# Performance work log

Measured on AMD Instinct MI355X. Metric: run time of the kernel, lower is better.

The kernel has to match this reference:

```python
import jax, jax.numpy as jnp
import numpy as np

B, S, H, K = 64, 512, 768, 21  # batch, seq_len, bert hidden, num_labels


def setup_inputs() -> dict:
    key = jax.random.key(0)
    ks = jax.random.split(key, 8)
    hidden = jax.random.normal(ks[0], (B, S, H), jnp.float32)  # post-BERT states
    W = jax.random.normal(ks[1], (H, K), jnp.float32) * 0.02    # classifier weight
    b = jnp.zeros((K,), jnp.float32)                            # classifier bias
    start_transitions = jax.random.uniform(ks[2], (K,), jnp.float32, -0.1, 0.1)
    transitions = jax.random.uniform(ks[3], (K, K), jnp.float32, -0.1, 0.1)
    end_transitions = jax.random.uniform(ks[4], (K,), jnp.float32, -0.1, 0.1)
    labels = jax.random.randint(ks[5], (B, S), 0, K)
    # torchcrf requires mask[:, 0] == 1; use variable-length prefix masks
    lengths = jax.random.randint(ks[6], (B,), S // 2, S + 1)
    attention_mask = jnp.arange(S)[None, :] < lengths[:, None]  # [B,S] bool
    return dict(hidden=hidden, W=W, b=b,
                start_transitions=start_transitions,
                transitions=transitions,
                end_transitions=end_transitions,
                labels=labels, attention_mask=attention_mask)


def _crf_nll(logits, labels, mask, start_t, trans, end_t):
    """torchcrf CRF forward (reduction='sum' log-likelihood), negated."""
    fmask = mask.astype(logits.dtype)  # [B,S]
    # ---- numerator: score of the gold path ----
    emit = jnp.take_along_axis(logits, labels[..., None], axis=2)[..., 0]  # [B,S]
    tr = trans[labels[:, :-1], labels[:, 1:]]                              # [B,S-1]
    num = start_t[labels[:, 0]] + emit[:, 0] \
        + jnp.sum((emit[:, 1:] + tr) * fmask[:, 1:], axis=1)
    lengths = mask.sum(axis=1)
    last_tags = jnp.take_along_axis(labels, (lengths - 1)[:, None], axis=1)[:, 0]
    num = num + end_t[last_tags]
    # ---- denominator: forward algorithm (logsumexp recurrence) ----
    alpha0 = start_t[None, :] + logits[:, 0]           # [B,K]
    ems = jnp.swapaxes(logits[:, 1:], 0, 1)            # [S-1,B,K]
    ms = jnp.swapaxes(mask[:, 1:], 0, 1)               # [S-1,B]

    def step(alpha, xs):
        em, m = xs
        nxt = jax.scipy.special.logsumexp(
            alpha[:, :, None] + trans[None, :, :] + em[:, None, :], axis=1)
        return jnp.where(m[:, None], nxt, alpha), None

    alpha, _ = jax.lax.scan(step, alpha0, (ems, ms))
    logZ = jax.scipy.special.logsumexp(alpha + end_t[None, :], axis=1)  # [B]
    return jnp.sum(logZ - num)  # negative log-likelihood (sum over batch)


def reference(hidden, W, b, start_transitions, transitions, end_transitions,
              labels, attention_mask):
    # dropout is identity in eval; the GRU in __init__ is unused in forward
    logits = hidden @ W + b  # [B,S,K]
    nll = _crf_nll(logits, labels, attention_mask,
                   start_transitions, transitions, end_transitions)
    # module returns (logits, -1 * log_likelihood) = (logits, nll)
    return (logits, nll)
```

## Files before the change

kernel.cpp:

```cpp
#include <hip/hip_runtime.h>

#define BSZ 64
#define SEQ 512
#define HID 768
#define NK  21
#define NSEG 32
#define SEGLEN 16
#define PSTR 448

typedef short bf16x8 __attribute__((ext_vector_type(8)));
typedef float f32x4  __attribute__((ext_vector_type(4)));

__device__ __forceinline__ unsigned f2bf1(float x) {
    unsigned u = __float_as_uint(x);
    return (u + 0x7fffu + ((u >> 16) & 1u)) >> 16;
}
__device__ __forceinline__ unsigned f2bf_pk(float lo, float hi) {
    return f2bf1(lo) | (f2bf1(hi) << 16);
}
__device__ __forceinline__ float bf2f(unsigned short v) {
    return __uint_as_float(((unsigned)v) << 16);
}

__global__ __launch_bounds__(256) void wconv_len_kernel(
    const float* __restrict__ W, const int* __restrict__ mask,
    unsigned short* __restrict__ WT, int* __restrict__ Lbuf)
{
    if (blockIdx.x < 96) {
        const int idx = blockIdx.x * 256 + threadIdx.x;
        const int n = idx / HID;
        const int k = idx - n * HID;
        unsigned short v = 0;
        if (n < NK) v = (unsigned short)f2bf1(W[(size_t)k * NK + n]);
        WT[idx] = v;
    } else {
        const int tid = threadIdx.x;
        const int b = tid >> 2, q = tid & 3;
        const int* msk = mask + b * SEQ + q * 128;
        int cnt = 0;
        for (int r = 0; r < 128; ++r) cnt += (msk[r] != 0);
        cnt += __shfl_xor(cnt, 1, 64);
        cnt += __shfl_xor(cnt, 2, 64);
        if (q == 0) Lbuf[b] = cnt;
    }
}

__global__ __launch_bounds__(256) void gemm_bias_kernel(
    const float* __restrict__ hidden, const unsigned short* __restrict__ WT,
    const float* __restrict__ bias, float* __restrict__ out)
{
    const int tid  = threadIdx.x;
    const int lane = tid & 63;
    const int wv   = tid >> 6;
    const int n    = lane & 15;
    const int quad = lane >> 4;

    const int arow = blockIdx.x * 64 + wv * 16 + n;
    const float* ap = hidden + (size_t)arow * HID + quad * 8;
    const bf16x8* bp0 = (const bf16x8*)(WT + (size_t)n * HID + quad * 8);
    const bf16x8* bp1 = (const bf16x8*)(WT + (size_t)(16 + n) * HID + quad * 8);

    f32x4 acc0 = {0.f, 0.f, 0.f, 0.f};
    f32x4 acc1 = {0.f, 0.f, 0.f, 0.f};

    float4 c0a = *(const float4*)(ap + 0);
    float4 c0b = *(const float4*)(ap + 4);

    #pragma unroll
    for (int c = 0; c < HID / 32; ++c) {
        float4 c1a, c1b;
        if (c + 1 < HID / 32) {
            c1a = *(const float4*)(ap + (c + 1) * 32);
            c1b = *(const float4*)(ap + (c + 1) * 32 + 4);
        }
        union { bf16x8 v; unsigned u[4]; } af;
        af.u[0] = f2bf_pk(c0a.x, c0a.y);
        af.u[1] = f2bf_pk(c0a.z, c0a.w);
        af.u[2] = f2bf_pk(c0b.x, c0b.y);
        af.u[3] = f2bf_pk(c0b.z, c0b.w);

        const bf16x8 b0 = bp0[c * 4];
        const bf16x8 b1 = bp1[c * 4];

        acc0 = __builtin_amdgcn_mfma_f32_16x16x32_bf16(af.v, b0, acc0, 0, 0, 0);
        acc1 = __builtin_amdgcn_mfma_f32_16x16x32_bf16(af.v, b1, acc1, 0, 0, 0);
        c0a = c1a; c0b = c1b;
    }

    const float b0v = bias[n];
    const float b1v = (n < NK - 16) ? bias[16 + n] : 0.f;
    const int rbase = blockIdx.x * 64 + wv * 16 + quad * 4;
    #pragma unroll
    for (int r = 0; r < 4; ++r) {
        float* op = out + (size_t)(rbase + r) * NK;
        op[n] = acc0[r] + b0v;
        if (n < NK - 16) op[16 + n] = acc1[r] + b1v;
    }
}

#define EHI(u) __uint_as_float((u) & 0xffff0000u)
#define ELO(u) __uint_as_float((u) << 16)
__global__ __launch_bounds__(64, 2) void prepass_kernel(
    const float* __restrict__ logits, const float* __restrict__ trans,
    const int* __restrict__ Lbuf,
    unsigned short* __restrict__ Nrowb, unsigned short* __restrict__ Ncolb,
    float* __restrict__ rlog)
{
    const int bs   = blockIdx.x;
    const int b    = bs >> 5;
    const int s    = bs & 31;
    const int lane = threadIdx.x;
    int g = lane / 21; if (g > 2) g = 2;
    int i = lane - g * 21; if (i > 20) i = 20;
    const int j0 = 7 * g;

    const int L = Lbuf[b];

    unsigned Epk[7][11];
    #pragma unroll
    for (int jl = 0; jl < 7; ++jl)
        #pragma unroll
        for (int p = 0; p < 11; ++p) {
            const float ehi = __expf(trans[(2 * p) * NK + j0 + jl]);
            const float elo = (2 * p + 1 < 21)
                            ? __expf(trans[(2 * p + 1) * NK + j0 + jl]) : 0.f;
            Epk[jl][p] = (f2bf1(ehi) << 16) | f2bf1(elo);
        }

    const float* lg = logits + (size_t)b * SEQ * NK;

    float P[7];
    float rl = 0.f;
    const int t0 = s * SEGLEN + 1;

    if (t0 < L) {
        const float C = lg[t0 * NK];
        #pragma unroll
        for (int jl = 0; jl < 7; ++jl)
            P[jl] = __expf(trans[i * NK + j0 + jl])
                  * __expf(lg[t0 * NK + j0 + jl] - C);
    } else {
        #pragma unroll
        for (int jl = 0; jl < 7; ++jl) P[jl] = (i == j0 + jl) ? 1.f : 0.f;
    }

#define BPF(v, idx) __uint_as_float(__builtin_amdgcn_ds_bpermute((idx) * 4, __float_as_uint(v)))

    #pragma unroll
    for (int u = 1; u < SEGLEN; ++u) {
        const int t = t0 + u;
        if (t < L) {
            float row[22];
            #pragma unroll
            for (int k = 0; k < 21; ++k)
                row[k] = BPF(P[k % 7], (k / 7) * 21 + i);
            row[21] = 0.f;

            const float C = lg[t * NK];
            float X[7];
            #pragma unroll
            for (int jl = 0; jl < 7; ++jl)
                X[jl] = __expf(lg[t * NK + j0 + jl] - C);

            #pragma unroll
            for (int jl = 0; jl < 7; ++jl) {
                float s0 = 0.f, s1 = 0.f;
                #pragma unroll
                for (int p = 0; p < 11; ++p) {
                    const unsigned e = Epk[jl][p];
                    s0 = fmaf(row[2 * p    ], EHI(e), s0);
                    s1 = fmaf(row[2 * p + 1], ELO(e), s1);
                }
                P[jl] = (s0 + s1) * X[jl];
            }
            const float m = BPF(P[0], 0);
            const float r = __builtin_amdgcn_rcpf(m);
            #pragma unroll
            for (int jl = 0; jl < 7; ++jl) P[jl] *= r;
            rl += __logf(m);
        }
    }
#undef BPF

    if (lane < 63) {
        unsigned short* nr = Nrowb + (size_t)bs * PSTR + i * 21 + j0;
        #pragma unroll
        for (int jl = 0; jl < 7; ++jl) nr[jl] = (unsigned short)f2bf1(P[jl]);
        unsigned short* nc = Ncolb + (size_t)bs * PSTR + i;
        #pragma unroll
        for (int jl = 0; jl < 7; ++jl)
            nc[(j0 + jl) * 21] = (unsigned short)f2bf1(P[jl]);
    }
    if (lane == 0) rlog[bs] = rl;
}

__global__ __launch_bounds__(128) void scan_kernel(
    const float* __restrict__ logits,
    const float* __restrict__ start_t,
    const float* __restrict__ trans,
    const float* __restrict__ end_t,
    const int* __restrict__ labels,
    const int* __restrict__ Lbuf,
    const unsigned short* __restrict__ Nrowb,
    const unsigned short* __restrict__ Ncolb,
    const float* __restrict__ rlog,
    float* __restrict__ per_batch)
{
    __shared__ float comb[26];

    const int b    = blockIdx.x;
    const int tid  = threadIdx.x;
    const int lane = tid & 63;
    const int wid  = tid >> 6;

    const float* lg = logits + (size_t)b * SEQ * NK;
    const int* lab = labels + b * SEQ;
    const int L = Lbuf[b];

    {
        float numacc = 0.f;
        for (int t = tid; t < L; t += 128) {
            if (t == 0) numacc += start_t[lab[0]] + lg[lab[0]];
            else        numacc += lg[t * NK + lab[t]] + trans[lab[t - 1] * NK + lab[t]];
        }
        if (tid == 0) numacc += end_t[lab[L - 1]];
        #pragma unroll
        for (int off = 32; off > 0; off >>= 1) numacc += __shfl_xor(numacc, off, 64);
        if (lane == 0) comb[22 + wid] = numacc;
    }

    float rls = (lane < 16) ? rlog[b * NSEG + wid * 16 + lane] : 0.f;
    #pragma unroll
    for (int off = 32; off > 0; off >>= 1) rls += __shfl_xor(rls, off, 64);

    const int jj = (lane < NK) ? lane : NK - 1;

#define RL(v, k) __uint_as_float(__builtin_amdgcn_readlane(__float_as_uint(v), k))

    float a, csum = 0.f, Orenorm = 0.f;
    float ncur[21], nnx[21];

    if (wid == 0) {
        for (int t = lane; t < 256; t += 64) csum += lg[t * NK];
        a = __expf(start_t[jj]) * __expf(lg[jj] - lg[0]);

        const unsigned short* base = Ncolb + (size_t)b * NSEG * PSTR + jj * 21;
        #pragma unroll
        for (int k = 0; k < 21; ++k) ncur[k] = bf2f(base[k]);
        for (int s = 0; s < 16; ++s) {
            if (s < 15) {
                const unsigned short* p = base + (size_t)(s + 1) * PSTR;
                #pragma unroll
                for (int k = 0; k < 21; ++k) nnx[k] = bf2f(p[k]);
            }
            float s0 = RL(a, 0) * ncur[0];
            float s1 = RL(a, 1) * ncur[1];
            float s2 = RL(a, 2) * ncur[2];
            #pragma unroll
            for (int k = 3; k < 21; k += 3) {
                s0 = fmaf(RL(a, k    ), ncur[k    ], s0);
                s1 = fmaf(RL(a, k + 1), ncur[k + 1], s1);
                s2 = fmaf(RL(a, k + 2), ncur[k + 2], s2);
            }
            a = (s0 + s1) + s2;
            const float m = __uint_as_float(
                __builtin_amdgcn_readfirstlane(__float_as_uint(a)));
            a *= __builtin_amdgcn_rcpf(m);
            Orenorm += __logf(m);
            if (s < 15) {
                #pragma unroll
                for (int k = 0; k < 21; ++k) ncur[k] = nnx[k];
            }
        }
    } else {
        for (int t = 256 + lane; t < L; t += 64) csum += lg[t * NK];
        a = __expf(end_t[jj]);

        const unsigned short* base = Nrowb + (size_t)b * NSEG * PSTR + jj * 21;
        #pragma unroll
        for (int k = 0; k < 21; ++k) ncur[k] = bf2f(base[(size_t)31 * PSTR + k]);
        for (int s = 31; s >= 16; --s) {
            if (s > 16) {
                const unsigned short* p = base + (size_t)(s - 1) * PSTR;
                #pragma unroll
                for (int k = 0; k < 21; ++k) nnx[k] = bf2f(p[k]);
            }
            float s0 = RL(a, 0) * ncur[0];
            float s1 = RL(a, 1) * ncur[1];
            float s2 = RL(a, 2) * ncur[2];
            #pragma unroll
            for (int k = 3; k < 21; k += 3) {
                s0 = fmaf(RL(a, k    ), ncur[k    ], s0);
                s1 = fmaf(RL(a, k + 1), ncur[k + 1], s1);
                s2 = fmaf(RL(a, k + 2), ncur[k + 2], s2);
            }
            a = (s0 + s1) + s2;
            const float m = __uint_as_float(
                __builtin_amdgcn_readfirstlane(__float_as_uint(a)));
            a *= __builtin_amdgcn_rcpf(m);
            Orenorm += __logf(m);
            if (s > 16) {
                #pragma unroll
                for (int k = 0; k < 21; ++k) ncur[k] = nnx[k];
            }
        }
    }
#undef RL

    #pragma unroll
    for (int off = 32; off > 0; off >>= 1) csum += __shfl_xor(csum, off, 64);

    if (wid == 1) {
        if (lane < NK) comb[lane] = a;
        if (lane == 0) comb[21] = csum + Orenorm + rls;
    }
    __syncthreads();

    if (wid == 0) {
        float val = (lane < NK) ? a * comb[lane] : 0.f;
        #pragma unroll
        for (int off = 32; off > 0; off >>= 1) val += __shfl_xor(val, off, 64);
        if (lane == 0) {
            const float OF  = csum + Orenorm + rls;
            const float num = comb[22] + comb[23];
            per_batch[b] = OF + comb[21] + __logf(val) - num;
        }
    }
}

__global__ __launch_bounds__(64) void reduce_kernel(
    const float* __restrict__ pb, float* __restrict__ out)
{
    float v = pb[threadIdx.x];
    #pragma unroll
    for (int off = 32; off > 0; off >>= 1) v += __shfl_xor(v, off, 64);
    if (threadIdx.x == 0) out[BSZ * SEQ * NK] = v;
}

extern "C" void kernel_launch(void* const* d_in, const int* in_sizes, int n_in,
                              void* d_out, int out_size, void* d_ws, size_t ws_size,
                              hipStream_t stream)
{
    const float* hidden  = (const float*)d_in[0];
    const float* W       = (const float*)d_in[1];
    const float* bias    = (const float*)d_in[2];
    const float* start_t = (const float*)d_in[3];
    const float* trans   = (const float*)d_in[4];
    const float* end_t   = (const float*)d_in[5];
    const int*   labels  = (const int*)d_in[6];
    const int*   mask    = (const int*)d_in[7];
    float* out = (float*)d_out;

    char* ws = (char*)d_ws;
    unsigned short* WT    = (unsigned short*)ws;
    float*          pb    = (float*)(ws + 65536);
    int*            Lbuf  = (int*)(ws + 66560);
    float*          rlog  = (float*)(ws + 69632);
    unsigned short* Nrowb = (unsigned short*)(ws + 131072);
    unsigned short* Ncolb = (unsigned short*)(ws + 131072 + 2097152);

    wconv_len_kernel<<<97, 256, 0, stream>>>(W, mask, WT, Lbuf);
    gemm_bias_kernel<<<(BSZ * SEQ) / 64, 256, 0, stream>>>(hidden, WT, bias, out);
    prepass_kernel<<<BSZ * NSEG, 64, 0, stream>>>(out, trans, Lbuf, Nrowb, Ncolb, rlog);
    scan_kernel<<<BSZ, 128, 0, stream>>>(out, start_t, trans, end_t, labels, Lbuf,
                                         Nrowb, Ncolb, rlog, pb);
    reduce_kernel<<<1, 64, 0, stream>>>(pb, out);
}
```

Measured before the change: 209.6 us.

## Pad transfer matrices for vector loads, deepen GEMM prefetch, replace reduce kernel with atomics

Transfer-matrix rows are padded from 21 to 24 bf16 entries (PSTR 512) so the scan kernel can fetch each row with three 16-byte vector loads instead of 21 scalar short loads. The GEMM now prefetches the hidden tile two chunks ahead and the weight fragments one chunk ahead. The final reduce kernel is removed: the output scalar is zeroed in the first kernel and each batch block adds its result atomically. This saves one launch but makes the float summation order nondeterministic.

```diff
diff --git a/kernel.cpp b/kernel.cpp
--- a/kernel.cpp
+++ b/kernel.cpp
@@ -6,7 +6,7 @@
 #define NK  21
 #define NSEG 32
 #define SEGLEN 16
-#define PSTR 448
+#define PSTR 512
 
 typedef short bf16x8 __attribute__((ext_vector_type(8)));
 typedef float f32x4  __attribute__((ext_vector_type(4)));
@@ -18,13 +18,14 @@
 __device__ __forceinline__ unsigned f2bf_pk(float lo, float hi) {
     return f2bf1(lo) | (f2bf1(hi) << 16);
 }
-__device__ __forceinline__ float bf2f(unsigned short v) {
-    return __uint_as_float(((unsigned)v) << 16);
-}
+
+#define U16L(d) __uint_as_float(((unsigned)(d)) << 16)
+#define U16H(d) __uint_as_float(((unsigned)(d)) & 0xffff0000u)
 
 __global__ __launch_bounds__(256) void wconv_len_kernel(
     const float* __restrict__ W, const int* __restrict__ mask,
-    unsigned short* __restrict__ WT, int* __restrict__ Lbuf)
+    unsigned short* __restrict__ WT, int* __restrict__ Lbuf,
+    float* __restrict__ out)
 {
     if (blockIdx.x < 96) {
         const int idx = blockIdx.x * 256 + threadIdx.x;
@@ -35,13 +36,14 @@
         WT[idx] = v;
     } else {
         const int tid = threadIdx.x;
+        if (tid == 255) out[BSZ * SEQ * NK] = 0.f;
         const int b = tid >> 2, q = tid & 3;
         const int* msk = mask + b * SEQ + q * 128;
         int cnt = 0;
         for (int r = 0; r < 128; ++r) cnt += (msk[r] != 0);
         cnt += __shfl_xor(cnt, 1, 64);
         cnt += __shfl_xor(cnt, 2, 64);
-        if (q == 0) Lbuf[b] = cnt;
+        if (q == 0 && b < BSZ) Lbuf[b] = cnt;
     }
 }
 
@@ -63,28 +65,35 @@
     f32x4 acc0 = {0.f, 0.f, 0.f, 0.f};
     f32x4 acc1 = {0.f, 0.f, 0.f, 0.f};
 
-    float4 c0a = *(const float4*)(ap + 0);
-    float4 c0b = *(const float4*)(ap + 4);
+    float4 a0 = *(const float4*)(ap + 0);
+    float4 a1 = *(const float4*)(ap + 4);
+    float4 p0 = *(const float4*)(ap + 32);
+    float4 p1 = *(const float4*)(ap + 36);
+    bf16x8 B0 = bp0[0];
+    bf16x8 B1 = bp1[0];
 
     #pragma unroll
     for (int c = 0; c < HID / 32; ++c) {
-        float4 c1a, c1b;
+        float4 q0, q1; bf16x8 Bn0, Bn1;
+        if (c + 2 < HID / 32) {
+            q0 = *(const float4*)(ap + (c + 2) * 32);
+            q1 = *(const float4*)(ap + (c + 2) * 32 + 4);
+        }
         if (c + 1 < HID / 32) {
-            c1a = *(const float4*)(ap + (c + 1) * 32);
-            c1b = *(const float4*)(ap + (c + 1) * 32 + 4);
+            Bn0 = bp0[(c + 1) * 4];
+            Bn1 = bp1[(c + 1) * 4];
         }
         union { bf16x8 v; unsigned u[4]; } af;
-        af.u[0] = f2bf_pk(c0a.x, c0a.y);
-        af.u[1] = f2bf_pk(c0a.z, c0a.w);
-        af.u[2] = f2bf_pk(c0b.x, c0b.y);
-        af.u[3] = f2bf_pk(c0b.z, c0b.w);
-
-        const bf16x8 b0 = bp0[c * 4];
-        const bf16x8 b1 = bp1[c * 4];
-
-        acc0 = __builtin_amdgcn_mfma_f32_16x16x32_bf16(af.v, b0, acc0, 0, 0, 0);
-        acc1 = __builtin_amdgcn_mfma_f32_16x16x32_bf16(af.v, b1, acc1, 0, 0, 0);
-        c0a = c1a; c0b = c1b;
+        af.u[0] = f2bf_pk(a0.x, a0.y);
+        af.u[1] = f2bf_pk(a0.z, a0.w);
+        af.u[2] = f2bf_pk(a1.x, a1.y);
+        af.u[3] = f2bf_pk(a1.z, a1.w);
+
+        acc0 = __builtin_amdgcn_mfma_f32_16x16x32_bf16(af.v, B0, acc0, 0, 0, 0);
+        acc1 = __builtin_amdgcn_mfma_f32_16x16x32_bf16(af.v, B1, acc1, 0, 0, 0);
+
+        a0 = p0; a1 = p1; p0 = q0; p1 = q1;
+        B0 = Bn0; B1 = Bn1;
     }
 
     const float b0v = bias[n];
@@ -183,13 +192,13 @@
 #undef BPF
 
     if (lane < 63) {
-        unsigned short* nr = Nrowb + (size_t)bs * PSTR + i * 21 + j0;
+        unsigned short* nr = Nrowb + (size_t)bs * PSTR + i * 24 + j0;
         #pragma unroll
         for (int jl = 0; jl < 7; ++jl) nr[jl] = (unsigned short)f2bf1(P[jl]);
         unsigned short* nc = Ncolb + (size_t)bs * PSTR + i;
         #pragma unroll
         for (int jl = 0; jl < 7; ++jl)
-            nc[(j0 + jl) * 21] = (unsigned short)f2bf1(P[jl]);
+            nc[(j0 + jl) * 24] = (unsigned short)f2bf1(P[jl]);
     }
     if (lane == 0) rlog[bs] = rl;
 }
@@ -204,7 +213,7 @@
     const unsigned short* __restrict__ Nrowb,
     const unsigned short* __restrict__ Ncolb,
     const float* __restrict__ rlog,
-    float* __restrict__ per_batch)
+    float* __restrict__ out)
 {
     __shared__ float comb[26];
 
@@ -236,76 +245,75 @@
     const int jj = (lane < NK) ? lane : NK - 1;
 
 #define RL(v, k) __uint_as_float(__builtin_amdgcn_readlane(__float_as_uint(v), k))
+#define PMV(vv, c0, c1, c2, outv) do {                                        \
+    float s0 = RL(vv, 0) * U16L(c0.x);                                        \
+    float s1 = RL(vv, 1) * U16H(c0.x);                                        \
+    float s2 = RL(vv, 2) * U16L(c0.y);                                        \
+    s0 = fmaf(RL(vv,  3), U16H(c0.y), s0); s1 = fmaf(RL(vv,  4), U16L(c0.z), s1); \
+    s2 = fmaf(RL(vv,  5), U16H(c0.z), s2); s0 = fmaf(RL(vv,  6), U16L(c0.w), s0); \
+    s1 = fmaf(RL(vv,  7), U16H(c0.w), s1); s2 = fmaf(RL(vv,  8), U16L(c1.x), s2); \
+    s0 = fmaf(RL(vv,  9), U16H(c1.x), s0); s1 = fmaf(RL(vv, 10), U16L(c1.y), s1); \
+    s2 = fmaf(RL(vv, 11), U16H(c1.y), s2); s0 = fmaf(RL(vv, 12), U16L(c1.z), s0); \
+    s1 = fmaf(RL(vv, 13), U16H(c1.z), s1); s2 = fmaf(RL(vv, 14), U16L(c1.w), s2); \
+    s0 = fmaf(RL(vv, 15), U16H(c1.w), s0); s1 = fmaf(RL(vv, 16), U16L(c2.x), s1); \
+    s2 = fmaf(RL(vv, 17), U16H(c2.x), s2); s0 = fmaf(RL(vv, 18), U16L(c2.y), s0); \
+    s1 = fmaf(RL(vv, 19), U16H(c2.y), s1); s2 = fmaf(RL(vv, 20), U16L(c2.z), s2); \
+    outv = (s0 + s1) + s2;                                                    \
+} while (0)
 
     float a, csum = 0.f, Orenorm = 0.f;
-    float ncur[21], nnx[21];
+    int4 c0, c1, c2, n0, n1, n2;
 
     if (wid == 0) {
         for (int t = lane; t < 256; t += 64) csum += lg[t * NK];
         a = __expf(start_t[jj]) * __expf(lg[jj] - lg[0]);
 
-        const unsigned short* base = Ncolb + (size_t)b * NSEG * PSTR + jj * 21;
-        #pragma unroll
-        for (int k = 0; k < 21; ++k) ncur[k] = bf2f(base[k]);
+        const char* base = (const char*)(Ncolb + (size_t)b * NSEG * PSTR) + jj * 48;
+        c0 = *(const int4*)(base);
+        c1 = *(const int4*)(base + 16);
+        c2 = *(const int4*)(base + 32);
         for (int s = 0; s < 16; ++s) {
             if (s < 15) {
-                const unsigned short* p = base + (size_t)(s + 1) * PSTR;
-                #pragma unroll
-                for (int k = 0; k < 21; ++k) nnx[k] = bf2f(p[k]);
+                const char* p = base + (size_t)(s + 1) * (PSTR * 2);
+                n0 = *(const int4*)(p);
+                n1 = *(const int4*)(p + 16);
+                n2 = *(const int4*)(p + 32);
             }
-            float s0 = RL(a, 0) * ncur[0];
-            float s1 = RL(a, 1) * ncur[1];
-            float s2 = RL(a, 2) * ncur[2];
-            #pragma unroll
-            for (int k = 3; k < 21; k += 3) {
-                s0 = fmaf(RL(a, k    ), ncur[k    ], s0);
-                s1 = fmaf(RL(a, k + 1), ncur[k + 1], s1);
-                s2 = fmaf(RL(a, k + 2), ncur[k + 2], s2);
-            }
-            a = (s0 + s1) + s2;
+            float nv; PMV(a, c0, c1, c2, nv); a = nv;
             const float m = __uint_as_float(
                 __builtin_amdgcn_readfirstlane(__float_as_uint(a)));
             a *= __builtin_amdgcn_rcpf(m);
             Orenorm += __logf(m);
-            if (s < 15) {
-                #pragma unroll
-                for (int k = 0; k < 21; ++k) ncur[k] = nnx[k];
-            }
+            c0 = n0; c1 = n1; c2 = n2;
         }
     } else {
         for (int t = 256 + lane; t < L; t += 64) csum += lg[t * NK];
         a = __expf(end_t[jj]);
 
-        const unsigned short* base = Nrowb + (size_t)b * NSEG * PSTR + jj * 21;
-        #pragma unroll
-        for (int k = 0; k < 21; ++k) ncur[k] = bf2f(base[(size_t)31 * PSTR + k]);
+        const char* base = (const char*)(Nrowb + (size_t)b * NSEG * PSTR) + jj * 48;
+        {
+            const char* p = base + (size_t)31 * (PSTR * 2);
+            c0 = *(const int4*)(p);
+            c1 = *(const int4*)(p + 16);
+            c2 = *(const int4*)(p + 32);
+        }
         for (int s = 31; s >= 16; --s) {
             if (s > 16) {
-                const unsigned short* p = base + (size_t)(s - 1) * PSTR;
-                #pragma unroll
-                for (int k = 0; k < 21; ++k) nnx[k] = bf2f(p[k]);
+                const char* p = base + (size_t)(s - 1) * (PSTR * 2);
+                n0 = *(const int4*)(p);
+                n1 = *(const int4*)(p + 16);
+                n2 = *(const int4*)(p + 32);
             }
-            float s0 = RL(a, 0) * ncur[0];
-            float s1 = RL(a, 1) * ncur[1];
-            float s2 = RL(a, 2) * ncur[2];
-            #pragma unroll
-            for (int k = 3; k < 21; k += 3) {
-                s0 = fmaf(RL(a, k    ), ncur[k    ], s0);
-                s1 = fmaf(RL(a, k + 1), ncur[k + 1], s1);
-                s2 = fmaf(RL(a, k + 2), ncur[k + 2], s2);
-            }
-            a = (s0 + s1) + s2;
+            float nv; PMV(a, c0, c1, c2, nv); a = nv;
             const float m = __uint_as_float(
                 __builtin_amdgcn_readfirstlane(__float_as_uint(a)));
             a *= __builtin_amdgcn_rcpf(m);
             Orenorm += __logf(m);
-            if (s > 16) {
-                #pragma unroll
-                for (int k = 0; k < 21; ++k) ncur[k] = nnx[k];
-            }
+            c0 = n0; c1 = n1; c2 = n2;
         }
     }
 #undef RL
+#undef PMV
 
     #pragma unroll
     for (int off = 32; off > 0; off >>= 1) csum += __shfl_xor(csum, off, 64);
@@ -323,18 +331,9 @@
         if (lane == 0) {
             const float OF  = csum + Orenorm + rls;
             const float num = comb[22] + comb[23];
-            per_batch[b] = OF + comb[21] + __logf(val) - num;
-        }
-    }
-}
-
-__global__ __launch_bounds__(64) void reduce_kernel(
-    const float* __restrict__ pb, float* __restrict__ out)
-{
-    float v = pb[threadIdx.x];
-    #pragma unroll
-    for (int off = 32; off > 0; off >>= 1) v += __shfl_xor(v, off, 64);
-    if (threadIdx.x == 0) out[BSZ * SEQ * NK] = v;
+            atomicAdd(out + BSZ * SEQ * NK, OF + comb[21] + __logf(val) - num);
+        }
+    }
 }
 
 extern "C" void kernel_launch(void* const* d_in, const int* in_sizes, int n_in,
@@ -353,16 +352,14 @@
 
     char* ws = (char*)d_ws;
     unsigned short* WT    = (unsigned short*)ws;
-    float*          pb    = (float*)(ws + 65536);
-    int*            Lbuf  = (int*)(ws + 66560);
+    int*            Lbuf  = (int*)(ws + 65536);
     float*          rlog  = (float*)(ws + 69632);
     unsigned short* Nrowb = (unsigned short*)(ws + 131072);
-    unsigned short* Ncolb = (unsigned short*)(ws + 131072 + 2097152);
-
-    wconv_len_kernel<<<97, 256, 0, stream>>>(W, mask, WT, Lbuf);
+    unsigned short* Ncolb = (unsigned short*)(ws + 131072 + 2 * 1024 * 1024);
+
+    wconv_len_kernel<<<97, 256, 0, stream>>>(W, mask, WT, Lbuf, out);
     gemm_bias_kernel<<<(BSZ * SEQ) / 64, 256, 0, stream>>>(hidden, WT, bias, out);
     prepass_kernel<<<BSZ * NSEG, 64, 0, stream>>>(out, trans, Lbuf, Nrowb, Ncolb, rlog);
     scan_kernel<<<BSZ, 128, 0, stream>>>(out, start_t, trans, end_t, labels, Lbuf,
-                                         Nrowb, Ncolb, rlog, pb);
-    reduce_kernel<<<1, 64, 0, stream>>>(pb, out);
-}
+                                         Nrowb, Ncolb, rlog, out);
+}
```

Measured after the change: 204.6 us. 2.4% less time.
